# Performance work log

Hardware: AMD Instinct MI355X
Metric: run time of the kernel (lower is better)

## Reference

```python
import jax, jax.numpy as jnp
import numpy as np

T, B, N, H, NT = 4096, 8, 256, 512, 5
W_SCALE = 0.02


def setup_inputs() -> dict:
    key = jax.random.key(0)
    ks = jax.random.split(key, 32)
    f32 = jnp.float32
    d = {}
    d['v_action'] = jax.random.normal(ks[0], (N, B, H), f32)
    d['v_frame'] = jax.random.normal(ks[1], (T, B, H), f32)
    d['v_task'] = jax.random.normal(ks[2], (NT, B, H), f32)
    d['v_mask'] = jax.random.randint(ks[3], (B, N), 0, 2, jnp.int32).at[:, 0].set(1)
    d['t_action'] = jax.random.normal(ks[4], (N, B, H), f32)
    d['t_frame'] = jax.random.normal(ks[5], (T, B, H), f32)
    d['t_task'] = jax.random.normal(ks[6], (NT, B, H), f32)
    d['t_mask'] = jax.random.randint(ks[7], (B, N), 0, 2, jnp.int32).at[:, 0].set(1)
    names = ['v_Wq', 'v_Wk', 'v_Wv', 'v_Wo', 't_Wq', 't_Wk', 't_Wv', 't_Wo']
    for i, nm in enumerate(names):
        d[nm] = jax.random.normal(ks[8 + i], (H, H), f32) * W_SCALE
    d['v_aw'] = jnp.asarray(0.1, f32)
    d['t_aw'] = jnp.asarray(0.1, f32)
    d['v_tw'] = jax.random.normal(ks[20], (H, 1), f32) * W_SCALE
    d['v_tb'] = jnp.zeros((1,), f32)
    d['t_tw'] = jax.random.normal(ks[21], (H, 1), f32) * W_SCALE
    d['t_tb'] = jnp.zeros((1,), f32)
    return d


def _compute_logit(frame, action, Wq, Wk):
    # frame: [T,B,H] queries, action: [N,B,H] keys -> logits [B,T,N]
    q = jnp.einsum('tbf,fh->tbh', frame, Wq)
    k = jnp.einsum('nba,ah->nbh', action, Wk)
    return jnp.einsum('tbh,nbh->btn', q, k) / jnp.sqrt(jnp.asarray(q.shape[-1], q.dtype))


def _compute_output(logit, alignment, action, frame, mask, Wv, Wo, aw):
    # shared detached cross-domain alignment, gated by sigmoid(alignment_weight)
    combined = logit + jax.nn.sigmoid(aw) * alignment          # [B,T,N]
    nomask = combined
    masked = jnp.where(mask[:, None, :] > 0, combined, -jnp.inf)
    attn = jax.nn.softmax(masked, axis=-1)                      # softmax over protos N
    v = jnp.einsum('nba,af->nbf', action, Wv)                   # values from protos
    out = jnp.einsum('btn,nbf->tbf', attn, v)
    out = jnp.einsum('tbf,fg->tbg', out, Wo) + frame            # residual to frames
    return out, nomask


def reference(v_action, v_frame, v_task, v_mask, t_action, t_frame, t_task, t_mask,
              v_Wq, v_Wk, v_Wv, v_Wo, v_aw, v_tw, v_tb,
              t_Wq, t_Wk, t_Wv, t_Wo, t_aw, t_tw, t_tb):
    v_logit = _compute_logit(v_frame, v_action, v_Wq, v_Wk)
    t_logit = _compute_logit(t_frame, t_action, t_Wq, t_Wk)
    v_share = jax.lax.stop_gradient(v_logit)
    t_share = jax.lax.stop_gradient(t_logit)
    v_out, v_nm = _compute_output(v_logit, t_share, v_action, v_frame, v_mask, v_Wv, v_Wo, v_aw)
    t_out, t_nm = _compute_output(t_logit, v_share, t_action, t_frame, t_mask, t_Wv, t_Wo, t_aw)
    v_ta = jnp.einsum('kbh,ho->kbo', v_task, v_tw) + v_tb       # [ntask,B,1]
    t_ta = jnp.einsum('kbh,ho->kbo', t_task, t_tw) + t_tb
    return (v_out, t_out,
            jnp.transpose(v_nm, (0, 2, 1)),                      # [B,N,T]
            jnp.transpose(t_nm, (0, 2, 1)),
            v_ta, t_ta)
```

## Files before the change

kernel.cpp:

```cpp
#include <hip/hip_runtime.h>
#include <hip/hip_bf16.h>
#include <cstddef>
#include <cstdint>

#define T_DIM 4096
#define B_DIM 8
#define N_DIM 256
#define H_DIM 512
#define NT_DIM 5

typedef __attribute__((ext_vector_type(8))) short short8;
typedef __attribute__((ext_vector_type(4))) float f32x4;

__device__ __forceinline__ short cvt_bf16(float f) {
  __hip_bfloat16 h = __float2bfloat16(f);
  union { __hip_bfloat16 h; short s; } u; u.h = h; return u.s;
}
__device__ __forceinline__ float bf2f(short s) {
  union { uint32_t u; float f; } v; v.u = ((uint32_t)(uint16_t)s) << 16;
  return v.f;
}

typedef __attribute__((address_space(1))) const void gvoid_t;
typedef __attribute__((address_space(3))) void lvoid_t;
__device__ __forceinline__ void gl_lds16(const void* g, void* lds_wave_base) {
  __builtin_amdgcn_global_load_lds((gvoid_t*)(uintptr_t)g,
                                   (lvoid_t*)(uint32_t)(uintptr_t)lds_wave_base,
                                   16, 0, 0);
}

#define MFMA16(a, b, c) __builtin_amdgcn_mfma_f32_16x16x32_bf16(a, b, c, 0, 0, 0)

struct GP {
  const void* A[4];
  const short* B[4];
  void* C[4];
  const float* R[4];
};

template<typename TA, typename TC, bool ADD_RES>
__global__ __launch_bounds__(256)
void gemm_tn(GP p, int zlog, long long a_bs, int lda,
             long long b_bs, int ldb, long long c_bs, int ldc,
             int K, float scale) {
  constexpr bool F32A = (sizeof(TA) == 4);
  constexpr int ASTR = F32A ? 40 : 32;
  constexpr int AB = 128 * ASTR * 2;
  constexpr int BB = 128 * 32 * 2;
  constexpr int HALF = AB + BB;
  constexpr int EPIB = 4 * 16 * 68 * 4;
  constexpr int BODYB = F32A ? (2 * AB + 3 * BB) : (3 * HALF);
  constexpr int SMEMB = BODYB > EPIB ? BODYB : EPIB;
  __shared__ __align__(16) char smem[SMEMB];

  const int tid  = threadIdx.x;
  const int lane = tid & 63;
  const int wave = tid >> 6;
  const int wr   = (wave >> 1) * 64;
  const int wc   = (wave & 1) * 64;
  const int lrow = lane & 15;
  const int kgrp = lane >> 4;

  const int dom = blockIdx.z >> zlog;
  const long long zz = blockIdx.z & ((1u << zlog) - 1u);

  const TA*    Abase = (const TA*)p.A[dom] + zz * a_bs + (long long)(blockIdx.x * 128) * lda;
  const short* Bbase = p.B[dom] + zz * b_bs + (long long)(blockIdx.y * 128) * ldb;

  const int ch_r  = lane >> 2;
  const int swcol = ((lane & 3) ^ (ch_r & 3)) * 8;
  const int srow = tid >> 1;
  const int scol = (tid & 1) * 16;

  f32x4 acc[4][4] = {};
  f32x4 pv[4];

  auto stageA_bf16 = [&](int buf, int k0) {
    short* As = (short*)(smem + buf * HALF);
    #pragma unroll
    for (int i = 0; i < 2; ++i) {
      const int c = wave + 4 * i;
      gl_lds16((const short*)Abase + (long long)(c * 16 + ch_r) * lda + k0 + swcol,
               &As[c * 512]);
    }
  };
  auto stageB_bf16 = [&](int buf, int k0) {
    short* Bs = (short*)(smem + buf * HALF + AB);
    #pragma unroll
    for (int i = 0; i < 2; ++i) {
      const int c = wave + 4 * i;
      gl_lds16(Bbase + (long long)(c * 16 + ch_r) * ldb + k0 + swcol, &Bs[c * 512]);
    }
  };
  auto stageB_f32p = [&](int buf, int k0) {
    short* Bs = (short*)(smem + 2 * AB + buf * BB);
    #pragma unroll
    for (int i = 0; i < 2; ++i) {
      const int c = wave + 4 * i;
      gl_lds16(Bbase + (long long)(c * 16 + ch_r) * ldb + k0 + swcol, &Bs[c * 512]);
    }
  };
  auto loadA_f32 = [&](int k0) {
    const float* gp = (const float*)Abase + (long long)srow * lda + k0 + scol;
    pv[0] = *(const f32x4*)(gp + 0);
    pv[1] = *(const f32x4*)(gp + 4);
    pv[2] = *(const f32x4*)(gp + 8);
    pv[3] = *(const f32x4*)(gp + 12);
  };
  auto writeA_f32 = [&](int buf) {
    short* As = (short*)(smem + buf * AB);
    short8 s0, s1;
    #pragma unroll
    for (int e = 0; e < 4; ++e) {
      s0[e]     = cvt_bf16(pv[0][e]);
      s0[4 + e] = cvt_bf16(pv[1][e]);
      s1[e]     = cvt_bf16(pv[2][e]);
      s1[4 + e] = cvt_bf16(pv[3][e]);
    }
    *(short8*)&As[srow * ASTR + scol]     = s0;
    *(short8*)&As[srow * ASTR + scol + 8] = s1;
  };
  auto compute = [&](int abuf, int bbuf) {
    const short* As = (const short*)(smem + (F32A ? abuf * AB : abuf * HALF));
    const short* Bs = (const short*)(smem + (F32A ? 2 * AB + bbuf * BB
                                                  : bbuf * HALF + AB));
    short8 af[4], bfr[4];
    const int u = kgrp ^ (lrow & 3);
    #pragma unroll
    for (int i = 0; i < 4; ++i) {
      const int row = wr + i * 16 + lrow;
      if constexpr (F32A) af[i] = *(const short8*)&As[row * ASTR + kgrp * 8];
      else                af[i] = *(const short8*)&As[row * 32 + u * 8];
    }
    #pragma unroll
    for (int j = 0; j < 4; ++j) {
      const int row = wc + j * 16 + lrow;
      bfr[j] = *(const short8*)&Bs[row * 32 + u * 8];
    }
    #pragma unroll
    for (int i = 0; i < 4; ++i)
      #pragma unroll
      for (int j = 0; j < 4; ++j)
        acc[i][j] = MFMA16(af[i], bfr[j], acc[i][j]);
  };

  const int NT = K >> 5;
  if constexpr (F32A) {
    loadA_f32(0); writeA_f32(0);
    stageB_f32p(0, 0);
    if (NT > 1) stageB_f32p(1, 32);
    if (NT > 1) loadA_f32(32);
    for (int t = 0; t < NT; ++t) {
      asm volatile("s_waitcnt lgkmcnt(0)" ::: "memory");
      __builtin_amdgcn_sched_barrier(0);
      __builtin_amdgcn_s_barrier();
      if (t + 2 < NT) stageB_f32p((t + 2) % 3, (t + 2) << 5);
      __builtin_amdgcn_sched_barrier(0);
      if (t + 2 < NT)      asm volatile("s_waitcnt vmcnt(8)" ::: "memory");
      else if (t + 1 < NT) asm volatile("s_waitcnt vmcnt(6)" ::: "memory");
      else                 asm volatile("s_waitcnt vmcnt(0)" ::: "memory");
      __builtin_amdgcn_sched_barrier(0);
      __builtin_amdgcn_s_barrier();
      __builtin_amdgcn_sched_barrier(0);
      compute(t & 1, t % 3);
      if (t + 1 < NT) writeA_f32((t + 1) & 1);
      if (t + 2 < NT) loadA_f32((t + 2) << 5);
    }
  } else {
    stageA_bf16(0, 0); stageB_bf16(0, 0);
    if (NT > 1) { stageA_bf16(1, 32); stageB_bf16(1, 32); }
    for (int t = 0; t < NT; ++t) {
      __builtin_amdgcn_s_barrier();
      if (t + 2 < NT) {
        stageA_bf16((t + 2) % 3, (t + 2) << 5);
        stageB_bf16((t + 2) % 3, (t + 2) << 5);
        __builtin_amdgcn_sched_barrier(0);
        asm volatile("s_waitcnt vmcnt(8)" ::: "memory");
      } else if (t + 1 < NT) {
        asm volatile("s_waitcnt vmcnt(4)" ::: "memory");
      } else {
        asm volatile("s_waitcnt vmcnt(0)" ::: "memory");
      }
      __builtin_amdgcn_sched_barrier(0);
      __builtin_amdgcn_s_barrier();
      __builtin_amdgcn_sched_barrier(0);
      compute(t % 3, t % 3);
    }
  }

  __syncthreads();
  float* myEp = (float*)smem + wave * (16 * 68);
  TC* Cd = (TC*)p.C[dom];
  const float* Res = p.R[dom];
  const long long cb = zz * c_bs;
  const int gm = blockIdx.x * 128 + wr;
  const int gn = blockIdx.y * 128 + wc;
  const int er = lane >> 2;
  const int ec = (lane & 3) * 16;

  f32x4 resA[4], resB[4];
  if constexpr (ADD_RES) {
    const long long b0 = cb + (long long)(gm + er) * ldc + gn + ec;
    #pragma unroll
    for (int q = 0; q < 4; ++q) resA[q] = *(const f32x4*)&Res[b0 + q * 4];
  }

  #pragma unroll
  for (int i = 0; i < 4; ++i) {
    if constexpr (ADD_RES) {
      if (i < 3) {
        const long long bn = cb + (long long)(gm + (i + 1) * 16 + er) * ldc + gn + ec;
        #pragma unroll
        for (int q = 0; q < 4; ++q) resB[q] = *(const f32x4*)&Res[bn + q * 4];
      }
    }
    #pragma unroll
    for (int j = 0; j < 4; ++j)
      #pragma unroll
      for (int r = 0; r < 4; ++r)
        myEp[(kgrp * 4 + r) * 68 + j * 16 + lrow] = acc[i][j][r];
    float vals[16];
    #pragma unroll
    for (int q = 0; q < 4; ++q) {
      f32x4 t4 = *(const f32x4*)&myEp[er * 68 + ec + q * 4];
      vals[q * 4 + 0] = t4[0]; vals[q * 4 + 1] = t4[1];
      vals[q * 4 + 2] = t4[2]; vals[q * 4 + 3] = t4[3];
    }
    const int row_g = gm + i * 16 + er;
    const long long base = cb + (long long)row_g * ldc + gn + ec;
    if constexpr (sizeof(TC) == 2) {
      short8 s0, s1;
      #pragma unroll
      for (int e = 0; e < 8; ++e) {
        s0[e] = cvt_bf16(vals[e] * scale);
        s1[e] = cvt_bf16(vals[8 + e] * scale);
      }
      *(short8*)&Cd[base]     = s0;
      *(short8*)&Cd[base + 8] = s1;
    } else {
      #pragma unroll
      for (int q = 0; q < 4; ++q) {
        f32x4 o;
        #pragma unroll
        for (int e = 0; e < 4; ++e) o[e] = vals[q * 4 + e] * scale;
        if constexpr (ADD_RES) {
          #pragma unroll
          for (int e = 0; e < 4; ++e) o[e] += resA[q][e];
        }
        *(f32x4*)&Cd[base + q * 4] = o;
      }
    }
    if constexpr (ADD_RES) {
      #pragma unroll
      for (int q = 0; q < 4; ++q) resA[q] = resB[q];
    }
  }
}

struct W6 { const float* p[6]; };

__global__ __launch_bounds__(256)
void rawcvt_kernel(W6 s, short* __restrict__ dst) {
  const int w = blockIdx.y;
  const float* src = s.p[w];
  short* d = dst + (long long)w * H_DIM * H_DIM;
  const int i = (blockIdx.x * 256 + threadIdx.x) * 8;
  f32x4 v0 = *(const f32x4*)(src + i);
  f32x4 v1 = *(const f32x4*)(src + i + 4);
  short8 o;
  #pragma unroll
  for (int e = 0; e < 4; ++e) { o[e] = cvt_bf16(v0[e]); o[4 + e] = cvt_bf16(v1[e]); }
  *(short8*)&d[i] = o;
}

struct W2 { const float* p[2]; };

__global__ __launch_bounds__(256)
void wtrans_kernel(W2 s, short* __restrict__ dst) {
  __shared__ float tile[32][33];
  const int w = blockIdx.z;
  const float* src = s.p[w];
  short* d = dst + (long long)w * H_DIM * H_DIM;
  const int tx = threadIdx.x, ty = threadIdx.y;
  const int n0 = blockIdx.x * 32, k0 = blockIdx.y * 32;
  #pragma unroll
  for (int i = 0; i < 4; ++i)
    tile[ty + 8 * i][tx] = src[(long long)(k0 + ty + 8 * i) * H_DIM + n0 + tx];
  __syncthreads();
  #pragma unroll
  for (int i = 0; i < 4; ++i)
    d[(long long)(n0 + ty + 8 * i) * H_DIM + k0 + tx] = cvt_bf16(tile[tx][ty + 8 * i]);
}

__global__ __launch_bounds__(256)
void ac16_kernel(const float* __restrict__ av, const float* __restrict__ at,
                 short* __restrict__ ov, short* __restrict__ ot) {
  const int dom = blockIdx.y;
  const float* src = dom ? at : av;
  short* d = dom ? ot : ov;
  const int i = (blockIdx.x * 256 + threadIdx.x) * 8;
  f32x4 v0 = *(const f32x4*)(src + i);
  f32x4 v1 = *(const f32x4*)(src + i + 4);
  short8 o;
  #pragma unroll
  for (int e = 0; e < 4; ++e) { o[e] = cvt_bf16(v0[e]); o[4 + e] = cvt_bf16(v1[e]); }
  *(short8*)&d[i] = o;
}

__global__ __launch_bounds__(256)
void softmax_fused(const short* __restrict__ Lv, const short* __restrict__ Lt,
                   const int* __restrict__ vmask, const int* __restrict__ tmask,
                   const float* __restrict__ vaw, const float* __restrict__ taw,
                   short* __restrict__ Av, short* __restrict__ At,
                   float* __restrict__ Onm_v, float* __restrict__ Onm_t) {
  __shared__ float tile[16 * 260];
  __shared__ int msk[2][256];
  const int tid = threadIdx.x;
  const int b = blockIdx.y, t0 = blockIdx.x * 16;
  const int r = tid >> 4, seg = tid & 15;
  msk[0][tid] = vmask[b * 256 + tid];
  msk[1][tid] = tmask[b * 256 + tid];
  __syncthreads();
  const float sv = 1.f / (1.f + __expf(-vaw[0]));
  const float st = 1.f / (1.f + __expf(-taw[0]));
  const long long off = ((long long)b * T_DIM + t0 + r) * N_DIM + seg * 16;

  short8 lv0 = *(const short8*)&Lv[off];
  short8 lv1 = *(const short8*)&Lv[off + 8];
  short8 lt0 = *(const short8*)&Lt[off];
  short8 lt1 = *(const short8*)&Lt[off + 8];
  float cv[16], ct[16];
  #pragma unroll
  for (int i = 0; i < 8; ++i) {
    float a0 = bf2f(lv0[i]), b0 = bf2f(lt0[i]);
    float a1 = bf2f(lv1[i]), b1 = bf2f(lt1[i]);
    cv[i]     = a0 + sv * b0;  ct[i]     = b0 + st * a0;
    cv[8 + i] = a1 + sv * b1;  ct[8 + i] = b1 + st * a1;
  }

#define EMIT_DOMAIN(CVAL, DI, AOUT, ONM) do {                                   \
    const int4 mA = *(const int4*)&msk[DI][seg * 16 + 0];                       \
    const int4 mB = *(const int4*)&msk[DI][seg * 16 + 4];                       \
    const int4 mC = *(const int4*)&msk[DI][seg * 16 + 8];                       \
    const int4 mD = *(const int4*)&msk[DI][seg * 16 + 12];                      \
    const int mk[16] = {mA.x, mA.y, mA.z, mA.w, mB.x, mB.y, mB.z, mB.w,         \
                        mC.x, mC.y, mC.z, mC.w, mD.x, mD.y, mD.z, mD.w};        \
    float mx = -3.4e38f;                                                        \
    _Pragma("unroll")                                                           \
    for (int q = 0; q < 16; ++q) if (mk[q] > 0) mx = fmaxf(mx, CVAL[q]);        \
    _Pragma("unroll")                                                           \
    for (int sh = 1; sh < 16; sh <<= 1) mx = fmaxf(mx, __shfl_xor(mx, sh));     \
    float ev[16]; float ssum = 0.f;                                             \
    _Pragma("unroll")                                                           \
    for (int q = 0; q < 16; ++q) {                                              \
      ev[q] = (mk[q] > 0) ? __expf(CVAL[q] - mx) : 0.f; ssum += ev[q];          \
    }                                                                           \
    _Pragma("unroll")                                                           \
    for (int sh = 1; sh < 16; sh <<= 1) ssum += __shfl_xor(ssum, sh);           \
    const float inv = 1.f / ssum;                                               \
    short8 o0, o1;                                                              \
    _Pragma("unroll")                                                           \
    for (int q = 0; q < 8; ++q) {                                               \
      o0[q] = cvt_bf16(ev[q] * inv); o1[q] = cvt_bf16(ev[8 + q] * inv);         \
    }                                                                           \
    *(short8*)&AOUT[off] = o0; *(short8*)&AOUT[off + 8] = o1;                   \
    _Pragma("unroll")                                                           \
    for (int q = 0; q < 4; ++q) {                                               \
      f32x4 tv; tv[0] = CVAL[q * 4]; tv[1] = CVAL[q * 4 + 1];                   \
      tv[2] = CVAL[q * 4 + 2]; tv[3] = CVAL[q * 4 + 3];                         \
      *(f32x4*)&tile[r * 260 + seg * 16 + q * 4] = tv;                          \
    }                                                                           \
    __syncthreads();                                                            \
    {                                                                           \
      float* obase = &ONM[((long long)b * N_DIM + tid) * T_DIM + t0];           \
      _Pragma("unroll")                                                         \
      for (int g = 0; g < 4; ++g) {                                             \
        f32x4 wv;                                                               \
        wv[0] = tile[(4 * g + 0) * 260 + tid];                                  \
        wv[1] = tile[(4 * g + 1) * 260 + tid];                                  \
        wv[2] = tile[(4 * g + 2) * 260 + tid];                                  \
        wv[3] = tile[(4 * g + 3) * 260 + tid];                                  \
        *(f32x4*)&obase[4 * g] = wv;                                            \
      }                                                                         \
    }                                                                           \
    __syncthreads();                                                            \
  } while (0)

  EMIT_DOMAIN(cv, 0, Av, Onm_v);
  EMIT_DOMAIN(ct, 1, At, Onm_t);
#undef EMIT_DOMAIN
}

__global__ __launch_bounds__(1024)
void task_kernel(const float* __restrict__ vtask, const float* __restrict__ ttask,
                 const float* __restrict__ vtw, const float* __restrict__ vtb,
                 const float* __restrict__ ttw, const float* __restrict__ ttb,
                 float* __restrict__ out_v, float* __restrict__ out_t) {
  const int wave = threadIdx.x >> 6;
  const int lane = threadIdx.x & 63;
  const int dom = wave >> 3;
  const int b   = wave & 7;
  const float* task = dom ? ttask : vtask;
  const float* tw   = dom ? ttw : vtw;
  const float  tb   = (dom ? ttb : vtb)[0];
  float* o = dom ? out_t : out_v;
  for (int k = 0; k < NT_DIM; ++k) {
    const float* row = task + ((long long)k * B_DIM + b) * H_DIM;
    float s = 0.f;
    for (int c = lane; c < H_DIM; c += 64) s += row[c] * tw[c];
    #pragma unroll
    for (int d = 32; d > 0; d >>= 1) s += __shfl_xor(s, d);
    if (lane == 0) o[k * B_DIM + b] = s + tb;
  }
}

extern "C" void kernel_launch(void* const* d_in, const int* in_sizes, int n_in,
                              void* d_out, int out_size, void* d_ws, size_t ws_size,
                              hipStream_t stream) {
  const float* v_action = (const float*)d_in[0];
  const float* v_frame  = (const float*)d_in[1];
  const float* v_task   = (const float*)d_in[2];
  const int*   v_mask   = (const int*)d_in[3];
  const float* t_action = (const float*)d_in[4];
  const float* t_frame  = (const float*)d_in[5];
  const float* t_task   = (const float*)d_in[6];
  const int*   t_mask   = (const int*)d_in[7];
  const float* v_aw = (const float*)d_in[16];
  const float* t_aw = (const float*)d_in[17];
  const float* v_tw = (const float*)d_in[18];
  const float* v_tb = (const float*)d_in[19];
  const float* t_tw = (const float*)d_in[20];
  const float* t_tb = (const float*)d_in[21];

  const long long TBH = (long long)T_DIM * B_DIM * H_DIM;
  const long long BTN = (long long)B_DIM * T_DIM * N_DIM;
  const long long WS  = (long long)H_DIM * H_DIM;

  float* out = (float*)d_out;
  float* out_v   = out;
  float* out_t   = out + TBH;
  float* out_vnm = out + 2 * TBH;
  float* out_tnm = out + 2 * TBH + BTN;
  float* out_vta = out + 2 * TBH + 2 * BTN;
  float* out_tta = out_vta + NT_DIM * B_DIM;

  char* w = (char*)d_ws;
  auto alloc = [&](long long bytes) {
    char* p = w; w += (bytes + 255) & ~255LL; return p;
  };
  short* WT    = (short*)alloc(8 * WS * 2);
  short* Mv    = (short*)alloc(WS * 2);
  short* Mt    = (short*)alloc(WS * 2);
  short* PTv   = (short*)alloc(WS * 2);
  short* PTt   = (short*)alloc(WS * 2);
  short* Ac16v = (short*)alloc(1048576LL * 2);
  short* Ac16t = (short*)alloc(1048576LL * 2);
  short* KWTv  = (short*)alloc(8LL * 131072 * 2);
  short* KWTt  = (short*)alloc(8LL * 131072 * 2);
  short* VWTv  = (short*)alloc(8LL * 131072 * 2);
  short* VWTt  = (short*)alloc(8LL * 131072 * 2);
  short* Av    = (short*)alloc(BTN * 2);
  short* At    = (short*)alloc(BTN * 2);
  short* Lv    = (short*)alloc(BTN * 2);
  short* Lt    = (short*)alloc(BTN * 2);

  const float rsq = 0.044194173824159216f;

  {
    W6 s6 = {{(const float*)d_in[8], (const float*)d_in[9], (const float*)d_in[10],
              (const float*)d_in[12], (const float*)d_in[13], (const float*)d_in[14]}};
    rawcvt_kernel<<<dim3(128, 6), dim3(256), 0, stream>>>(s6, WT);
    W2 s2 = {{(const float*)d_in[11], (const float*)d_in[15]}};
    wtrans_kernel<<<dim3(16, 16, 2), dim3(32, 8), 0, stream>>>(s2, WT + 6 * WS);
  }

  ac16_kernel<<<dim3(512, 2), dim3(256), 0, stream>>>(v_action, t_action, Ac16v, Ac16t);

  {
    GP p = {{WT + 0 * WS, WT + 3 * WS, WT + 6 * WS, WT + 7 * WS},
            {WT + 1 * WS, WT + 4 * WS, WT + 2 * WS, WT + 5 * WS},
            {Mv, Mt, PTv, PTt},
            {nullptr, nullptr, nullptr, nullptr}};
    gemm_tn<short, short, false><<<dim3(4, 4, 4), dim3(256), 0, stream>>>(
        p, 0, 0LL, H_DIM, 0LL, H_DIM, 0LL, H_DIM, 512, 1.f);
  }

  {
    GP p = {{Ac16v, Ac16t}, {Mv, Mt}, {KWTv, KWTt}, {nullptr, nullptr}};
    gemm_tn<short, short, false><<<dim3(2, 4, 16), dim3(256), 0, stream>>>(
        p, 3, 512LL, B_DIM * H_DIM, 0LL, H_DIM, 131072LL, H_DIM, 512, 1.f);
  }

  {
    GP p = {{PTv, PTt}, {Ac16v, Ac16t}, {VWTv, VWTt}, {nullptr, nullptr}};
    gemm_tn<short, short, false><<<dim3(4, 2, 16), dim3(256), 0, stream>>>(
        p, 3, 0LL, H_DIM, 512LL, B_DIM * H_DIM, 131072LL, N_DIM, 512, 1.f);
  }

  {
    GP p = {{v_frame, t_frame}, {KWTv, KWTt}, {Lv, Lt}, {nullptr, nullptr}};
    gemm_tn<float, short, false><<<dim3(32, 2, 16), dim3(256), 0, stream>>>(
        p, 3, 512LL, B_DIM * H_DIM, 131072LL, H_DIM,
        (long long)T_DIM * N_DIM, N_DIM, 512, rsq);
  }

  softmax_fused<<<dim3(T_DIM / 16, B_DIM), dim3(256), 0, stream>>>(
      Lv, Lt, v_mask, t_mask, v_aw, t_aw, Av, At, out_vnm, out_tnm);

  {
    GP p = {{Av, At}, {VWTv, VWTt}, {out_v, out_t}, {v_frame, t_frame}};
    gemm_tn<short, float, true><<<dim3(32, 4, 16), dim3(256), 0, stream>>>(
        p, 3, (long long)T_DIM * N_DIM, N_DIM, 131072LL, N_DIM,
        512LL, B_DIM * H_DIM, 256, 1.f);
  }

  task_kernel<<<dim3(1), dim3(1024), 0, stream>>>(
      v_task, t_task, v_tw, v_tb, t_tw, t_tb, out_vta, out_tta);
}
```

Baseline: 246.0 us.

## Merge prep kernels and batch K/V projection GEMMs into one launch

The three weight/action conversion kernels and the task-head kernel are folded into a single prep kernel that dispatches on block index. The two independent small GEMMs, action×M for keys and PT×action for values, are combined into one grouped launch. Per-domain strides and grid limits are passed in the parameter struct so each launch can mix shapes, and out-of-range blocks exit early. This cuts launch count and lets small grids share the GPU, at the cost of some idle blocks and extra per-block parameter loads.

```diff
diff --git a/kernel.cpp b/kernel.cpp
--- a/kernel.cpp
+++ b/kernel.cpp
@@ -36,13 +36,14 @@
   const short* B[4];
   void* C[4];
   const float* R[4];
+  long long a_bs[4], b_bs[4], c_bs[4];
+  int lda[4], ldb[4], ldc[4];
+  int xlim[4], ylim[4];
 };
 
 template<typename TA, typename TC, bool ADD_RES>
 __global__ __launch_bounds__(256)
-void gemm_tn(GP p, int zlog, long long a_bs, int lda,
-             long long b_bs, int ldb, long long c_bs, int ldc,
-             int K, float scale) {
+void gemm_tn(GP p, int zlog, int K, float scale) {
   constexpr bool F32A = (sizeof(TA) == 4);
   constexpr int ASTR = F32A ? 40 : 32;
   constexpr int AB = 128 * ASTR * 2;
@@ -53,6 +54,12 @@
   constexpr int SMEMB = BODYB > EPIB ? BODYB : EPIB;
   __shared__ __align__(16) char smem[SMEMB];
 
+  const int dom = blockIdx.z >> zlog;
+  const long long zz = blockIdx.z & ((1u << zlog) - 1u);
+  if ((int)blockIdx.x >= p.xlim[dom] || (int)blockIdx.y >= p.ylim[dom]) return;
+
+  const int lda = p.lda[dom], ldb = p.ldb[dom], ldc = p.ldc[dom];
+
   const int tid  = threadIdx.x;
   const int lane = tid & 63;
   const int wave = tid >> 6;
@@ -61,11 +68,10 @@
   const int lrow = lane & 15;
   const int kgrp = lane >> 4;
 
-  const int dom = blockIdx.z >> zlog;
-  const long long zz = blockIdx.z & ((1u << zlog) - 1u);
-
-  const TA*    Abase = (const TA*)p.A[dom] + zz * a_bs + (long long)(blockIdx.x * 128) * lda;
-  const short* Bbase = p.B[dom] + zz * b_bs + (long long)(blockIdx.y * 128) * ldb;
+  const TA*    Abase = (const TA*)p.A[dom] + zz * p.a_bs[dom] +
+                       (long long)(blockIdx.x * 128) * lda;
+  const short* Bbase = p.B[dom] + zz * p.b_bs[dom] +
+                       (long long)(blockIdx.y * 128) * ldb;
 
   const int ch_r  = lane >> 2;
   const int swcol = ((lane & 3) ^ (ch_r & 3)) * 8;
@@ -192,7 +198,7 @@
   float* myEp = (float*)smem + wave * (16 * 68);
   TC* Cd = (TC*)p.C[dom];
   const float* Res = p.R[dom];
-  const long long cb = zz * c_bs;
+  const long long cb = zz * p.c_bs[dom];
   const int gm = blockIdx.x * 128 + wr;
   const int gn = blockIdx.y * 128 + wc;
   const int er = lane >> 2;
@@ -257,54 +263,84 @@
   }
 }
 
-struct W6 { const float* p[6]; };
+struct PrepArgs {
+  const float* w6[6];
+  const float* w2[2];
+  const float* av; const float* at;
+  const float* vtask; const float* ttask;
+  const float* vtw; const float* vtb;
+  const float* ttw; const float* ttb;
+  short* WT; short* Ac16v; short* Ac16t;
+  float* out_vta; float* out_tta;
+};
 
 __global__ __launch_bounds__(256)
-void rawcvt_kernel(W6 s, short* __restrict__ dst) {
-  const int w = blockIdx.y;
-  const float* src = s.p[w];
-  short* d = dst + (long long)w * H_DIM * H_DIM;
-  const int i = (blockIdx.x * 256 + threadIdx.x) * 8;
-  f32x4 v0 = *(const f32x4*)(src + i);
-  f32x4 v1 = *(const f32x4*)(src + i + 4);
-  short8 o;
-  #pragma unroll
-  for (int e = 0; e < 4; ++e) { o[e] = cvt_bf16(v0[e]); o[4 + e] = cvt_bf16(v1[e]); }
-  *(short8*)&d[i] = o;
-}
-
-struct W2 { const float* p[2]; };
-
-__global__ __launch_bounds__(256)
-void wtrans_kernel(W2 s, short* __restrict__ dst) {
+void prep_kernel(PrepArgs a) {
   __shared__ float tile[32][33];
-  const int w = blockIdx.z;
-  const float* src = s.p[w];
-  short* d = dst + (long long)w * H_DIM * H_DIM;
-  const int tx = threadIdx.x, ty = threadIdx.y;
-  const int n0 = blockIdx.x * 32, k0 = blockIdx.y * 32;
-  #pragma unroll
-  for (int i = 0; i < 4; ++i)
-    tile[ty + 8 * i][tx] = src[(long long)(k0 + ty + 8 * i) * H_DIM + n0 + tx];
-  __syncthreads();
-  #pragma unroll
-  for (int i = 0; i < 4; ++i)
-    d[(long long)(n0 + ty + 8 * i) * H_DIM + k0 + tx] = cvt_bf16(tile[tx][ty + 8 * i]);
-}
-
-__global__ __launch_bounds__(256)
-void ac16_kernel(const float* __restrict__ av, const float* __restrict__ at,
-                 short* __restrict__ ov, short* __restrict__ ot) {
-  const int dom = blockIdx.y;
-  const float* src = dom ? at : av;
-  short* d = dom ? ot : ov;
-  const int i = (blockIdx.x * 256 + threadIdx.x) * 8;
-  f32x4 v0 = *(const f32x4*)(src + i);
-  f32x4 v1 = *(const f32x4*)(src + i + 4);
-  short8 o;
-  #pragma unroll
-  for (int e = 0; e < 4; ++e) { o[e] = cvt_bf16(v0[e]); o[4 + e] = cvt_bf16(v1[e]); }
-  *(short8*)&d[i] = o;
+  const long long WS = (long long)H_DIM * H_DIM;
+  const int bx = blockIdx.x;
+  const int tid = threadIdx.x;
+
+  if (bx < 768) {
+    const int w = bx >> 7;
+    const int blk = bx & 127;
+    const float* src = a.w6[w];
+    short* d = a.WT + (long long)w * WS;
+    const int i = (blk * 256 + tid) * 8;
+    f32x4 v0 = *(const f32x4*)(src + i);
+    f32x4 v1 = *(const f32x4*)(src + i + 4);
+    short8 o;
+    #pragma unroll
+    for (int e = 0; e < 4; ++e) { o[e] = cvt_bf16(v0[e]); o[4 + e] = cvt_bf16(v1[e]); }
+    *(short8*)&d[i] = o;
+  } else if (bx < 1280) {
+    const int r = bx - 768;
+    const int w = r >> 8;
+    const int rem = r & 255;
+    const int n0 = (rem >> 4) * 32, k0 = (rem & 15) * 32;
+    const float* src = a.w2[w];
+    short* d = a.WT + (long long)(6 + w) * WS;
+    const int tx = tid & 31, ty = tid >> 5;
+    #pragma unroll
+    for (int i = 0; i < 4; ++i)
+      tile[ty + 8 * i][tx] = src[(long long)(k0 + ty + 8 * i) * H_DIM + n0 + tx];
+    __syncthreads();
+    #pragma unroll
+    for (int i = 0; i < 4; ++i)
+      d[(long long)(n0 + ty + 8 * i) * H_DIM + k0 + tx] = cvt_bf16(tile[tx][ty + 8 * i]);
+  } else if (bx < 2304) {
+    const int r = bx - 1280;
+    const int dom = r >> 9;
+    const int blk = r & 511;
+    const float* src = dom ? a.at : a.av;
+    short* d = dom ? a.Ac16t : a.Ac16v;
+    const int i = (blk * 256 + tid) * 8;
+    f32x4 v0 = *(const f32x4*)(src + i);
+    f32x4 v1 = *(const f32x4*)(src + i + 4);
+    short8 o;
+    #pragma unroll
+    for (int e = 0; e < 4; ++e) { o[e] = cvt_bf16(v0[e]); o[4 + e] = cvt_bf16(v1[e]); }
+    *(short8*)&d[i] = o;
+  } else {
+    const int wave = tid >> 6;
+    const int lane = tid & 63;
+    for (int g = wave; g < 16; g += 4) {
+      const int dom = g >> 3;
+      const int b = g & 7;
+      const float* task = dom ? a.ttask : a.vtask;
+      const float* tw   = dom ? a.ttw : a.vtw;
+      const float  tb   = (dom ? a.ttb : a.vtb)[0];
+      float* o = dom ? a.out_tta : a.out_vta;
+      for (int k = 0; k < NT_DIM; ++k) {
+        const float* row = task + ((long long)k * B_DIM + b) * H_DIM;
+        float s = 0.f;
+        for (int c = lane; c < H_DIM; c += 64) s += row[c] * tw[c];
+        #pragma unroll
+        for (int d = 32; d > 0; d >>= 1) s += __shfl_xor(s, d);
+        if (lane == 0) o[k * B_DIM + b] = s + tb;
+      }
+    }
+  }
 }
 
 __global__ __launch_bounds__(256)
@@ -391,29 +427,6 @@
 #undef EMIT_DOMAIN
 }
 
-__global__ __launch_bounds__(1024)
-void task_kernel(const float* __restrict__ vtask, const float* __restrict__ ttask,
-                 const float* __restrict__ vtw, const float* __restrict__ vtb,
-                 const float* __restrict__ ttw, const float* __restrict__ ttb,
-                 float* __restrict__ out_v, float* __restrict__ out_t) {
-  const int wave = threadIdx.x >> 6;
-  const int lane = threadIdx.x & 63;
-  const int dom = wave >> 3;
-  const int b   = wave & 7;
-  const float* task = dom ? ttask : vtask;
-  const float* tw   = dom ? ttw : vtw;
-  const float  tb   = (dom ? ttb : vtb)[0];
-  float* o = dom ? out_t : out_v;
-  for (int k = 0; k < NT_DIM; ++k) {
-    const float* row = task + ((long long)k * B_DIM + b) * H_DIM;
-    float s = 0.f;
-    for (int c = lane; c < H_DIM; c += 64) s += row[c] * tw[c];
-    #pragma unroll
-    for (int d = 32; d > 0; d >>= 1) s += __shfl_xor(s, d);
-    if (lane == 0) o[k * B_DIM + b] = s + tb;
-  }
-}
-
 extern "C" void kernel_launch(void* const* d_in, const int* in_sizes, int n_in,
                               void* d_out, int out_size, void* d_ws, size_t ws_size,
                               hipStream_t stream) {
@@ -467,53 +480,84 @@
   const float rsq = 0.044194173824159216f;
 
   {
-    W6 s6 = {{(const float*)d_in[8], (const float*)d_in[9], (const float*)d_in[10],
-              (const float*)d_in[12], (const float*)d_in[13], (const float*)d_in[14]}};
-    rawcvt_kernel<<<dim3(128, 6), dim3(256), 0, stream>>>(s6, WT);
-    W2 s2 = {{(const float*)d_in[11], (const float*)d_in[15]}};
-    wtrans_kernel<<<dim3(16, 16, 2), dim3(32, 8), 0, stream>>>(s2, WT + 6 * WS);
-  }
-
-  ac16_kernel<<<dim3(512, 2), dim3(256), 0, stream>>>(v_action, t_action, Ac16v, Ac16t);
+    PrepArgs a;
+    a.w6[0] = (const float*)d_in[8];  a.w6[1] = (const float*)d_in[9];
+    a.w6[2] = (const float*)d_in[10]; a.w6[3] = (const float*)d_in[12];
+    a.w6[4] = (const float*)d_in[13]; a.w6[5] = (const float*)d_in[14];
+    a.w2[0] = (const float*)d_in[11]; a.w2[1] = (const float*)d_in[15];
+    a.av = v_action; a.at = t_action;
+    a.vtask = v_task; a.ttask = t_task;
+    a.vtw = v_tw; a.vtb = v_tb; a.ttw = t_tw; a.ttb = t_tb;
+    a.WT = WT; a.Ac16v = Ac16v; a.Ac16t = Ac16t;
+    a.out_vta = out_vta; a.out_tta = out_tta;
+    prep_kernel<<<dim3(2305), dim3(256), 0, stream>>>(a);
+  }
 
   {
-    GP p = {{WT + 0 * WS, WT + 3 * WS, WT + 6 * WS, WT + 7 * WS},
-            {WT + 1 * WS, WT + 4 * WS, WT + 2 * WS, WT + 5 * WS},
-            {Mv, Mt, PTv, PTt},
-            {nullptr, nullptr, nullptr, nullptr}};
+    GP p = {};
+    const short* As[4] = {WT + 0 * WS, WT + 3 * WS, WT + 6 * WS, WT + 7 * WS};
+    const short* Bs[4] = {WT + 1 * WS, WT + 4 * WS, WT + 2 * WS, WT + 5 * WS};
+    short* Cs[4] = {Mv, Mt, PTv, PTt};
+    for (int s = 0; s < 4; ++s) {
+      p.A[s] = As[s]; p.B[s] = Bs[s]; p.C[s] = Cs[s]; p.R[s] = nullptr;
+      p.a_bs[s] = 0; p.b_bs[s] = 0; p.c_bs[s] = 0;
+      p.lda[s] = H_DIM; p.ldb[s] = H_DIM; p.ldc[s] = H_DIM;
+      p.xlim[s] = 4; p.ylim[s] = 4;
+    }
     gemm_tn<short, short, false><<<dim3(4, 4, 4), dim3(256), 0, stream>>>(
-        p, 0, 0LL, H_DIM, 0LL, H_DIM, 0LL, H_DIM, 512, 1.f);
+        p, 0, 512, 1.f);
   }
 
   {
-    GP p = {{Ac16v, Ac16t}, {Mv, Mt}, {KWTv, KWTt}, {nullptr, nullptr}};
-    gemm_tn<short, short, false><<<dim3(2, 4, 16), dim3(256), 0, stream>>>(
-        p, 3, 512LL, B_DIM * H_DIM, 0LL, H_DIM, 131072LL, H_DIM, 512, 1.f);
+    GP p = {};
+    p.A[0] = Ac16v; p.B[0] = Mv; p.C[0] = KWTv;
+    p.A[1] = Ac16t; p.B[1] = Mt; p.C[1] = KWTt;
+    for (int s = 0; s < 2; ++s) {
+      p.a_bs[s] = 512; p.lda[s] = B_DIM * H_DIM;
+      p.b_bs[s] = 0;   p.ldb[s] = H_DIM;
+      p.c_bs[s] = 131072; p.ldc[s] = H_DIM;
+      p.xlim[s] = 2; p.ylim[s] = 4; p.R[s] = nullptr;
+    }
+    p.A[2] = PTv; p.B[2] = Ac16v; p.C[2] = VWTv;
+    p.A[3] = PTt; p.B[3] = Ac16t; p.C[3] = VWTt;
+    for (int s = 2; s < 4; ++s) {
+      p.a_bs[s] = 0;   p.lda[s] = H_DIM;
+      p.b_bs[s] = 512; p.ldb[s] = B_DIM * H_DIM;
+      p.c_bs[s] = 131072; p.ldc[s] = N_DIM;
+      p.xlim[s] = 4; p.ylim[s] = 2; p.R[s] = nullptr;
+    }
+    gemm_tn<short, short, false><<<dim3(4, 4, 32), dim3(256), 0, stream>>>(
+        p, 3, 512, 1.f);
   }
 
   {
-    GP p = {{PTv, PTt}, {Ac16v, Ac16t}, {VWTv, VWTt}, {nullptr, nullptr}};
-    gemm_tn<short, short, false><<<dim3(4, 2, 16), dim3(256), 0, stream>>>(
-        p, 3, 0LL, H_DIM, 512LL, B_DIM * H_DIM, 131072LL, N_DIM, 512, 1.f);
-  }
-
-  {
-    GP p = {{v_frame, t_frame}, {KWTv, KWTt}, {Lv, Lt}, {nullptr, nullptr}};
+    GP p = {};
+    p.A[0] = v_frame; p.B[0] = KWTv; p.C[0] = Lv;
+    p.A[1] = t_frame; p.B[1] = KWTt; p.C[1] = Lt;
+    for (int s = 0; s < 2; ++s) {
+      p.a_bs[s] = 512; p.lda[s] = B_DIM * H_DIM;
+      p.b_bs[s] = 131072; p.ldb[s] = H_DIM;
+      p.c_bs[s] = (long long)T_DIM * N_DIM; p.ldc[s] = N_DIM;
+      p.xlim[s] = 32; p.ylim[s] = 2; p.R[s] = nullptr;
+    }
     gemm_tn<float, short, false><<<dim3(32, 2, 16), dim3(256), 0, stream>>>(
-        p, 3, 512LL, B_DIM * H_DIM, 131072LL, H_DIM,
-        (long long)T_DIM * N_DIM, N_DIM, 512, rsq);
+        p, 3, 512, rsq);
   }
 
   softmax_fused<<<dim3(T_DIM / 16, B_DIM), dim3(256), 0, stream>>>(
       Lv, Lt, v_mask, t_mask, v_aw, t_aw, Av, At, out_vnm, out_tnm);
 
   {
-    GP p = {{Av, At}, {VWTv, VWTt}, {out_v, out_t}, {v_frame, t_frame}};
+    GP p = {};
+    p.A[0] = Av; p.B[0] = VWTv; p.C[0] = out_v; p.R[0] = v_frame;
+    p.A[1] = At; p.B[1] = VWTt; p.C[1] = out_t; p.R[1] = t_frame;
+    for (int s = 0; s < 2; ++s) {
+      p.a_bs[s] = (long long)T_DIM * N_DIM; p.lda[s] = N_DIM;
+      p.b_bs[s] = 131072; p.ldb[s] = N_DIM;
+      p.c_bs[s] = 512; p.ldc[s] = B_DIM * H_DIM;
+      p.xlim[s] = 32; p.ylim[s] = 4;
+    }
     gemm_tn<short, float, true><<<dim3(32, 4, 16), dim3(256), 0, stream>>>(
-        p, 3, (long long)T_DIM * N_DIM, N_DIM, 131072LL, N_DIM,
-        512LL, B_DIM * H_DIM, 256, 1.f);
-  }
-
-  task_kernel<<<dim3(1), dim3(1024), 0, stream>>>(
-      v_task, t_task, v_tw, v_tb, t_tw, t_tb, out_vta, out_tta);
-}
+        p, 3, 256, 1.f);
+  }
+}
```

Result: slower. 277.7 us (+12.9%).
